# Optimization experiments

Measured on AMD Instinct MI355X. Metric: run time of the kernel, lower is better.

The kernel has to match this reference:

```python
import jax, jax.numpy as jnp
import numpy as np

B, D_IN, N_EXP, D_EXP, TOP_K = 8192, 1024, 8, 1024, 2


def setup_inputs() -> dict:
    key = jax.random.key(0)
    ks = jax.random.split(key, 6)
    s_in = 1.0 / np.sqrt(D_IN)
    s_exp = 1.0 / np.sqrt(D_EXP)
    return {
        "x": jax.random.normal(ks[0], (B, D_IN), jnp.float32),
        "gate_w": jax.random.normal(ks[1], (D_IN, N_EXP), jnp.float32) * s_in,
        "w1": jax.random.normal(ks[2], (N_EXP, D_IN, D_EXP), jnp.float32) * s_in,
        "b1": jax.random.normal(ks[3], (N_EXP, D_EXP), jnp.float32) * 0.01,
        "w2": jax.random.normal(ks[4], (N_EXP, D_EXP, D_EXP), jnp.float32) * s_exp,
        "b2": jax.random.normal(ks[5], (N_EXP, D_EXP), jnp.float32) * 0.01,
    }


def _moe(x, gate_w, w1, b1, w2, b2):
    # Gating: top-k sparse softmax over expert logits.
    gate_logits = x @ gate_w                          # (B, E)
    top_vals, top_idx = jax.lax.top_k(gate_logits, TOP_K)  # (B, K)
    # softmax over only the top-k logits == softmax of -inf-scattered logits
    top_w = jax.nn.softmax(top_vals, axis=-1)          # (B, K)
    gate_weights = jnp.zeros_like(gate_logits).at[
        jnp.arange(x.shape[0])[:, None], top_idx
    ].set(top_w)                                       # (B, E)
    # Dense all-expert MLP (matches torch.stack over experts).
    h = jax.nn.gelu(jnp.einsum("bd,edf->ebf", x, w1) + b1[:, None, :],
                    approximate=False)                 # (E, B, F)
    expert_outs = jnp.einsum("ebf,efg->ebg", h, w2) + b2[:, None, :]  # (E, B, G)
    output = jnp.einsum("be,ebg->bg", gate_weights, expert_outs)      # (B, G)
    return output, gate_weights


def reference(x, gate_w, w1, b1, w2, b2):
    return _moe(x, gate_w, w1, b1, w2, b2)
```

## Files before the change

kernel.cpp:

```cpp
#include <hip/hip_runtime.h>
#include <math.h>
#include <stdint.h>


#define NTOK   8192
#define DIN    1024
#define NEXP   8
#define DEXP   1024
#define MAXROWS 17408
#define MAXTILES 136

typedef __bf16 bf16x8_t __attribute__((ext_vector_type(8)));
typedef float f32x4 __attribute__((ext_vector_type(4)));

__device__ __forceinline__ unsigned short f2bf(float f) {
  union { float f; unsigned int u; } v; v.f = f;
  unsigned int u = v.u;
  u += 0x7fffu + ((u >> 16) & 1u);
  return (unsigned short)(u >> 16);
}

__device__ __forceinline__ float bf2f(unsigned short s) {
  union { unsigned int u; float f; } v; v.u = ((unsigned int)s) << 16;
  return v.f;
}

__device__ __forceinline__ void async16(const void* g, void* l) {
  __builtin_amdgcn_global_load_lds((const __attribute__((address_space(1))) void*)g,
                                   (__attribute__((address_space(3))) void*)l, 16, 0, 0);
}

__device__ __forceinline__ float gelu_fast(float v) {
  float u = v * (1.5957691216057308f + 0.07135481627f * v * v);
  return v * (1.0f / (1.0f + __expf(-u)));
}

__global__ __launch_bounds__(256) void gate_cast_kernel(const float* __restrict__ x,
                                                        const float* __restrict__ gw,
                                                        unsigned short* __restrict__ xbf,
                                                        float* __restrict__ outGate,
                                                        int* __restrict__ topE,
                                                        float* __restrict__ topW,
                                                        int* __restrict__ rowTok) {
  int b = blockIdx.x;
  int tid = threadIdx.x;
  if (b >= 2048) {
    int base = (b - 2048) * 1024 + tid * 4;
    *(int4*)(rowTok + base) = make_int4(-1, -1, -1, -1);
    return;
  }
  __shared__ float gwT[NEXP][1024];
  #pragma unroll
  for (int it = 0; it < 8; ++it) {
    int idx = it * 256 + tid;
    int fk = idx >> 1;
    int e0 = (idx & 1) * 4;
    float4 g = *(const float4*)(gw + fk * 8 + e0);
    gwT[e0 + 0][fk] = g.x; gwT[e0 + 1][fk] = g.y;
    gwT[e0 + 2][fk] = g.z; gwT[e0 + 3][fk] = g.w;
  }
  __syncthreads();

  int lane = tid & 63, wv = tid >> 6;
  int t = b * 4 + wv;
  const float4* xr = (const float4*)(x + (size_t)t * 1024);
  ushort4* xo = (ushort4*)(xbf + (size_t)t * 1024);
  double acc[NEXP];
  #pragma unroll
  for (int e = 0; e < NEXP; ++e) acc[e] = 0.0;
  #pragma unroll
  for (int j = 0; j < 4; ++j) {
    int q = lane + 64 * j;
    float4 v = xr[q];
    ushort4 r;
    r.x = f2bf(v.x); r.y = f2bf(v.y); r.z = f2bf(v.z); r.w = f2bf(v.w);
    xo[q] = r;
    float vv[4] = {v.x, v.y, v.z, v.w};
    #pragma unroll
    for (int e = 0; e < NEXP; ++e) {
      float4 g = *(const float4*)&gwT[e][4 * q];
      acc[e] += (double)vv[0] * (double)g.x;
      acc[e] += (double)vv[1] * (double)g.y;
      acc[e] += (double)vv[2] * (double)g.z;
      acc[e] += (double)vv[3] * (double)g.w;
    }
  }
  #pragma unroll
  for (int off = 32; off > 0; off >>= 1) {
    #pragma unroll
    for (int e = 0; e < NEXP; ++e) acc[e] += __shfl_xor(acc[e], off);
  }
  if (lane == 0) {
    int e0 = 0; double v0 = acc[0];
    #pragma unroll
    for (int e = 1; e < NEXP; ++e) if (acc[e] > v0) { v0 = acc[e]; e0 = e; }
    int e1 = -1; double v1 = -1e300;
    #pragma unroll
    for (int e = 0; e < NEXP; ++e) if (e != e0 && acc[e] > v1) { v1 = acc[e]; e1 = e; }
    float ex = expf((float)(v1 - v0));
    float inv = 1.0f / (1.0f + ex);
    float w0 = inv, w1v = ex * inv;
    float g8[8];
    #pragma unroll
    for (int e = 0; e < NEXP; ++e) g8[e] = 0.f;
    g8[e0] = w0; g8[e1] = w1v;
    float4* gp = (float4*)(outGate + t * 8);
    gp[0] = *(float4*)&g8[0];
    gp[1] = *(float4*)&g8[4];
    topE[t * 2 + 0] = e0; topE[t * 2 + 1] = e1;
    topW[t * 2 + 0] = w0; topW[t * 2 + 1] = w1v;
  }
}

__global__ __launch_bounds__(1024) void slot_kernel(const int* __restrict__ topE,
                                                    int* __restrict__ topRow,
                                                    int* __restrict__ rowTok,
                                                    int* __restrict__ tileExpert,
                                                    int* __restrict__ tileRowBase,
                                                    const float* __restrict__ w1,
                                                    unsigned short* __restrict__ w1T) {
  __shared__ int wtot[16][NEXP];
  __shared__ int wbase[16][NEXP];
  __shared__ int soff[NEXP];
  __shared__ float tile[64 * 65];
  int tid = threadIdx.x;
  if (blockIdx.x != 0) {
    int idx = blockIdx.x - 1;
    int e = idx >> 8, rest = idx & 255, kt = rest >> 4, nt = rest & 15;
    const float* s = w1 + (size_t)e * DIN * DEXP + (size_t)kt * 64 * 1024 + nt * 64;
    unsigned short* d = w1T + (size_t)e * DIN * DEXP + (size_t)nt * 64 * 1024 + kt * 64;
    int a = tid & 15, r = tid >> 4;
    float4 v = *(const float4*)(s + (size_t)r * 1024 + a * 4);
    tile[r * 65 + a * 4 + 0] = v.x;
    tile[r * 65 + a * 4 + 1] = v.y;
    tile[r * 65 + a * 4 + 2] = v.z;
    tile[r * 65 + a * 4 + 3] = v.w;
    __syncthreads();
    int nr = r;
    ushort4 o;
    o.x = f2bf(tile[(a * 4 + 0) * 65 + nr]);
    o.y = f2bf(tile[(a * 4 + 1) * 65 + nr]);
    o.z = f2bf(tile[(a * 4 + 2) * 65 + nr]);
    o.w = f2bf(tile[(a * 4 + 3) * 65 + nr]);
    *(ushort4*)(d + (size_t)nr * 1024 + a * 4) = o;
    return;
  }
  int lane = tid & 63, wv = tid >> 6;
  int a0 = tid * 16;
  unsigned long long pk = 0ull;
  int cnt[NEXP];
  #pragma unroll
  for (int e = 0; e < NEXP; ++e) cnt[e] = 0;
  for (int i = 0; i < 16; ++i) {
    int e = topE[a0 + i];
    pk |= (unsigned long long)e << (i * 4);
    cnt[e]++;
  }
  int excl[NEXP];
  #pragma unroll
  for (int e = 0; e < NEXP; ++e) {
    int v = cnt[e], sum = v;
    #pragma unroll
    for (int d = 1; d < 64; d <<= 1) {
      int u = __shfl_up(sum, d);
      if (lane >= d) sum += u;
    }
    excl[e] = sum - v;
    if (lane == 63) wtot[wv][e] = sum;
  }
  __syncthreads();
  if (tid == 0) {
    int counts[NEXP];
    for (int e = 0; e < NEXP; ++e) {
      int s = 0;
      for (int w = 0; w < 16; ++w) { wbase[w][e] = s; s += wtot[w][e]; }
      counts[e] = s;
    }
    int row = 0, tile2 = 0;
    for (int e = 0; e < NEXP; ++e) {
      soff[e] = row;
      int nt = (counts[e] + 127) >> 7;
      for (int i = 0; i < nt; ++i) { tileExpert[tile2] = e; tileRowBase[tile2] = row + i * 128; ++tile2; }
      row += nt << 7;
    }
    for (; tile2 < MAXTILES; ++tile2) tileExpert[tile2] = -1;
  }
  __syncthreads();
  int base[NEXP], run[NEXP];
  #pragma unroll
  for (int e = 0; e < NEXP; ++e) { base[e] = soff[e] + wbase[wv][e] + excl[e]; run[e] = 0; }
  for (int i = 0; i < 16; ++i) {
    int e = (int)((pk >> (i * 4)) & 7ull);
    int row = base[e] + run[e]++;
    rowTok[row] = (a0 + i) >> 1;
    topRow[a0 + i] = row;
  }
}

__global__ __launch_bounds__(256) void gemm1_kernel(const unsigned short* __restrict__ xbf,
                                                    const unsigned short* __restrict__ w1T,
                                                    const float* __restrict__ b1,
                                                    const float* __restrict__ w2,
                                                    unsigned short* __restrict__ w2T,
                                                    const int* __restrict__ tileExpert,
                                                    const int* __restrict__ tileRowBase,
                                                    const int* __restrict__ rowTok,
                                                    unsigned short* __restrict__ h) {
  __shared__ __align__(16) unsigned short sm[128 * 64 * 2];
  int bid = blockIdx.x;
  int tid = threadIdx.x;
  if (bid < 2048) {
    float* tile = (float*)sm;
    int e = bid >> 8, rest = bid & 255, kt = rest >> 4, nt = rest & 15;
    const float* s = w2 + (size_t)e * DEXP * DEXP + (size_t)kt * 64 * 1024 + nt * 64;
    unsigned short* d = w2T + (size_t)e * DEXP * DEXP + (size_t)nt * 64 * 1024 + kt * 64;
    int a = tid & 15, r0 = tid >> 4;
    #pragma unroll
    for (int p = 0; p < 4; ++p) {
      int r = r0 + p * 16;
      float4 v = *(const float4*)(s + (size_t)r * 1024 + a * 4);
      tile[r * 65 + a * 4 + 0] = v.x;
      tile[r * 65 + a * 4 + 1] = v.y;
      tile[r * 65 + a * 4 + 2] = v.z;
      tile[r * 65 + a * 4 + 3] = v.w;
    }
    __syncthreads();
    #pragma unroll
    for (int p = 0; p < 4; ++p) {
      int nr = r0 + p * 16;
      ushort4 o;
      o.x = f2bf(tile[(a * 4 + 0) * 65 + nr]);
      o.y = f2bf(tile[(a * 4 + 1) * 65 + nr]);
      o.z = f2bf(tile[(a * 4 + 2) * 65 + nr]);
      o.w = f2bf(tile[(a * 4 + 3) * 65 + nr]);
      *(ushort4*)(d + (size_t)nr * 1024 + a * 4) = o;
    }
    return;
  }
  int g = bid - 2048;
  int tileId = g % MAXTILES;
  int e = tileExpert[tileId];
  if (e < 0) return;
  int rowBase = tileRowBase[tileId];
  int n0 = (g / MAXTILES) * 128;
  unsigned short* sA = sm;
  unsigned short* sB = sm + 128 * 64;
  int lane = tid & 63, wv = tid >> 6;
  int srow = tid >> 3;
  int scolSw = (((tid & 7) ^ ((tid >> 3) & 7)) * 8);
  int tok[4];
  #pragma unroll
  for (int i = 0; i < 4; ++i) {
    int tk = rowTok[rowBase + srow + i * 32];
    tok[i] = tk < 0 ? 0 : tk;
  }
  const unsigned short* Bmat = w1T + (size_t)e * DIN * DEXP;
  int wm = ((tid >> 6) & 1) * 64, wn = (tid >> 7) * 64;
  int rsel = lane & 15, q = lane >> 4;
  int rk = rsel & 7;
  f32x4 acc[4][4] = {};
  for (int kk = 0; kk < DIN; kk += 64) {
    #pragma unroll
    for (int i = 0; i < 4; ++i) {
      int abase = __builtin_amdgcn_readfirstlane((wv * 8 + i * 32) * 128);
      async16(xbf + (size_t)tok[i] * 1024 + kk + scolSw, (char*)sm + abase);
      async16(Bmat + (size_t)(n0 + srow + i * 32) * 1024 + kk + scolSw,
              (char*)sm + abase + 16384);
    }
    __syncthreads();
    #pragma unroll
    for (int ks = 0; ks < 64; ks += 32) {
      int co = (((ks >> 3) + q) ^ rk) * 8;
      bf16x8_t af[4], bfr[4];
      #pragma unroll
      for (int mi = 0; mi < 4; ++mi)
        af[mi] = *(const bf16x8_t*)&sA[(wm + mi * 16 + rsel) * 64 + co];
      #pragma unroll
      for (int ni = 0; ni < 4; ++ni)
        bfr[ni] = *(const bf16x8_t*)&sB[(wn + ni * 16 + rsel) * 64 + co];
      #pragma unroll
      for (int mi = 0; mi < 4; ++mi)
        #pragma unroll
        for (int ni = 0; ni < 4; ++ni)
          acc[mi][ni] = __builtin_amdgcn_mfma_f32_16x16x32_bf16(af[mi], bfr[ni], acc[mi][ni], 0, 0, 0);
    }
    __syncthreads();
  }
  float b1v[4];
  int quad = lane >> 4;
  #pragma unroll
  for (int ni = 0; ni < 4; ++ni) b1v[ni] = b1[e * 1024 + n0 + wn + ni * 16 + rsel];
  #pragma unroll
  for (int mi = 0; mi < 4; ++mi)
    #pragma unroll
    for (int ni = 0; ni < 4; ++ni)
      #pragma unroll
      for (int r = 0; r < 4; ++r) {
        int m = wm + mi * 16 + quad * 4 + r;
        int n = wn + ni * 16 + rsel;
        sm[m * 128 + n] = f2bf(gelu_fast(acc[mi][ni][r] + b1v[ni]));
      }
  __syncthreads();
  #pragma unroll
  for (int i = 0; i < 8; ++i) {
    int idx = i * 2048 + tid * 8;
    int m = idx >> 7, c = idx & 127;
    int gg = rowBase + m;
    *(uint4*)(h + (size_t)gg * 1024 + n0 + c) = *(const uint4*)&sm[idx];
  }
}

__global__ __launch_bounds__(256) void gemm2_kernel(const unsigned short* __restrict__ h,
                                                    const unsigned short* __restrict__ w2T,
                                                    const float* __restrict__ b2,
                                                    const int* __restrict__ tileExpert,
                                                    const int* __restrict__ tileRowBase,
                                                    unsigned short* __restrict__ y) {
  int tileId = blockIdx.x;
  int e = tileExpert[tileId];
  if (e < 0) return;
  int rowBase = tileRowBase[tileId];
  int n0 = blockIdx.y * 128;
  __shared__ __align__(16) unsigned short sm[128 * 64 * 2];
  unsigned short* sA = sm;
  unsigned short* sB = sm + 128 * 64;
  int tid = threadIdx.x, lane = tid & 63, wv = tid >> 6;
  int srow = tid >> 3;
  int scolSw = (((tid & 7) ^ ((tid >> 3) & 7)) * 8);
  const unsigned short* Bmat = w2T + (size_t)e * DEXP * DEXP;
  int wm = ((tid >> 6) & 1) * 64, wn = (tid >> 7) * 64;
  int rsel = lane & 15, q = lane >> 4;
  int rk = rsel & 7;
  f32x4 acc[4][4] = {};
  for (int kk = 0; kk < DEXP; kk += 64) {
    #pragma unroll
    for (int i = 0; i < 4; ++i) {
      int abase = __builtin_amdgcn_readfirstlane((wv * 8 + i * 32) * 128);
      async16(h + (size_t)(rowBase + srow + i * 32) * 1024 + kk + scolSw, (char*)sm + abase);
      async16(Bmat + (size_t)(n0 + srow + i * 32) * 1024 + kk + scolSw,
              (char*)sm + abase + 16384);
    }
    __syncthreads();
    #pragma unroll
    for (int ks = 0; ks < 64; ks += 32) {
      int co = (((ks >> 3) + q) ^ rk) * 8;
      bf16x8_t af[4], bfr[4];
      #pragma unroll
      for (int mi = 0; mi < 4; ++mi)
        af[mi] = *(const bf16x8_t*)&sA[(wm + mi * 16 + rsel) * 64 + co];
      #pragma unroll
      for (int ni = 0; ni < 4; ++ni)
        bfr[ni] = *(const bf16x8_t*)&sB[(wn + ni * 16 + rsel) * 64 + co];
      #pragma unroll
      for (int mi = 0; mi < 4; ++mi)
        #pragma unroll
        for (int ni = 0; ni < 4; ++ni)
          acc[mi][ni] = __builtin_amdgcn_mfma_f32_16x16x32_bf16(af[mi], bfr[ni], acc[mi][ni], 0, 0, 0);
    }
    __syncthreads();
  }
  float b2v[4];
  int quad = lane >> 4;
  #pragma unroll
  for (int ni = 0; ni < 4; ++ni) b2v[ni] = b2[e * 1024 + n0 + wn + ni * 16 + rsel];
  #pragma unroll
  for (int mi = 0; mi < 4; ++mi)
    #pragma unroll
    for (int ni = 0; ni < 4; ++ni)
      #pragma unroll
      for (int r = 0; r < 4; ++r) {
        int m = wm + mi * 16 + quad * 4 + r;
        int n = wn + ni * 16 + rsel;
        sm[m * 128 + n] = f2bf(acc[mi][ni][r] + b2v[ni]);
      }
  __syncthreads();
  #pragma unroll
  for (int i = 0; i < 8; ++i) {
    int idx = i * 2048 + tid * 8;
    int m = idx >> 7, c = idx & 127;
    int g = rowBase + m;
    *(uint4*)(y + (size_t)g * 1024 + n0 + c) = *(const uint4*)&sm[idx];
  }
}

__global__ __launch_bounds__(256) void combine_kernel(const unsigned short* __restrict__ y,
                                                      const int* __restrict__ topRow,
                                                      const float* __restrict__ topW,
                                                      float* __restrict__ out) {
  int tid = threadIdx.x;
  int wv = tid >> 6, lane = tid & 63;
  int t = blockIdx.x * 4 + wv;
  int r0 = topRow[t * 2 + 0], r1 = topRow[t * 2 + 1];
  float w0 = topW[t * 2 + 0], w1 = topW[t * 2 + 1];
  const unsigned short* p0 = y + (size_t)r0 * 1024 + lane * 16;
  const unsigned short* p1 = y + (size_t)r1 * 1024 + lane * 16;
  float* op = out + (size_t)t * 1024 + lane * 16;
  #pragma unroll
  for (int hh = 0; hh < 2; ++hh) {
    union { uint4 v; unsigned short s[8]; } a, b;
    a.v = *(const uint4*)(p0 + hh * 8);
    b.v = *(const uint4*)(p1 + hh * 8);
    float o[8];
    #pragma unroll
    for (int j = 0; j < 8; ++j)
      o[j] = w0 * bf2f(a.s[j]) + w1 * bf2f(b.s[j]);
    *(float4*)(op + hh * 8) = *(float4*)&o[0];
    *(float4*)(op + hh * 8 + 4) = *(float4*)&o[4];
  }
}

extern "C" void kernel_launch(void* const* d_in, const int* in_sizes, int n_in,
                              void* d_out, int out_size, void* d_ws, size_t ws_size,
                              hipStream_t stream) {
  const float* x  = (const float*)d_in[0];
  const float* gw = (const float*)d_in[1];
  const float* w1 = (const float*)d_in[2];
  const float* b1 = (const float*)d_in[3];
  const float* w2 = (const float*)d_in[4];
  const float* b2 = (const float*)d_in[5];
  float* out = (float*)d_out;

  char* ws = (char*)d_ws;
  int* tileExpert  = (int*)ws;
  int* tileRowBase = tileExpert + MAXTILES;
  int* topE        = tileRowBase + MAXTILES;
  int* topRow      = topE + 16384;
  float* topW      = (float*)(topRow + 16384);
  int* rowTok      = (int*)(ws + (256 << 10));
  unsigned short* xbf  = (unsigned short*)(ws + (512 << 10));
  unsigned short* w1T  = xbf + (size_t)NTOK * DIN;
  unsigned short* w2T  = w1T + (size_t)NEXP * DIN * DEXP;
  unsigned short* hbuf = w2T + (size_t)NEXP * DEXP * DEXP;
  unsigned short* ybuf = hbuf + (size_t)MAXROWS * DEXP;

  gate_cast_kernel<<<2048 + 17, 256, 0, stream>>>(x, gw, xbf,
                                                  out + (size_t)NTOK * DEXP,
                                                  topE, topW, rowTok);
  slot_kernel<<<1 + 2048, 1024, 0, stream>>>(topE, topRow, rowTok, tileExpert,
                                             tileRowBase, w1, w1T);
  gemm1_kernel<<<2048 + MAXTILES * 8, 256, 0, stream>>>(xbf, w1T, b1, w2, w2T,
                                                        tileExpert, tileRowBase,
                                                        rowTok, hbuf);
  gemm2_kernel<<<dim3(MAXTILES, 8), 256, 0, stream>>>(hbuf, w2T, b2, tileExpert,
                                                      tileRowBase, ybuf);
  combine_kernel<<<NTOK / 4, 256, 0, stream>>>(ybuf, topRow, topW, out);
}
```

Baseline: 292.3 us.

## Use 256x256 double-buffered MFMA tiles for both expert GEMMs and move w2 cast

Replaces the two 128x128 single-buffered grouped GEMMs with one templated 512-thread kernel on 256x256 tiles. It double-buffers LDS through async global-to-LDS loads with explicit waitcnt, and raises MFMA priority with s_setprio. Expert row padding moves to 256-row tiles, and the w2 transpose/cast moves into the gate kernel so the GEMM launch does only matrix work. Bigger tiles improve reuse but pad more rows per expert and launch far fewer blocks (72x4), which can leave the GPU's compute units underused.

```diff
diff --git a/kernel.cpp b/kernel.cpp
--- a/kernel.cpp
+++ b/kernel.cpp
@@ -7,8 +7,8 @@
 #define DIN    1024
 #define NEXP   8
 #define DEXP   1024
-#define MAXROWS 17408
-#define MAXTILES 136
+#define MAXROWS 18432
+#define MAXT   72
 
 typedef __bf16 bf16x8_t __attribute__((ext_vector_type(8)));
 typedef float f32x4 __attribute__((ext_vector_type(4)));
@@ -37,19 +37,51 @@
 
 __global__ __launch_bounds__(256) void gate_cast_kernel(const float* __restrict__ x,
                                                         const float* __restrict__ gw,
+                                                        const float* __restrict__ w2,
                                                         unsigned short* __restrict__ xbf,
+                                                        unsigned short* __restrict__ w2T,
                                                         float* __restrict__ outGate,
                                                         int* __restrict__ topE,
                                                         float* __restrict__ topW,
                                                         int* __restrict__ rowTok) {
+  __shared__ __align__(16) char smem[32768];
   int b = blockIdx.x;
   int tid = threadIdx.x;
-  if (b >= 2048) {
-    int base = (b - 2048) * 1024 + tid * 4;
+  if (b >= 4096) {
+    int base = (b - 4096) * 1024 + tid * 4;
     *(int4*)(rowTok + base) = make_int4(-1, -1, -1, -1);
     return;
   }
-  __shared__ float gwT[NEXP][1024];
+  if (b >= 2048) {
+    float* tile = (float*)smem;
+    int idx = b - 2048;
+    int e = idx >> 8, rest = idx & 255, kt = rest >> 4, nt = rest & 15;
+    const float* s = w2 + (size_t)e * DEXP * DEXP + (size_t)kt * 64 * 1024 + nt * 64;
+    unsigned short* d = w2T + (size_t)e * DEXP * DEXP + (size_t)nt * 64 * 1024 + kt * 64;
+    int a = tid & 15, r0 = tid >> 4;
+    #pragma unroll
+    for (int p = 0; p < 4; ++p) {
+      int r = r0 + p * 16;
+      float4 v = *(const float4*)(s + (size_t)r * 1024 + a * 4);
+      tile[r * 65 + a * 4 + 0] = v.x;
+      tile[r * 65 + a * 4 + 1] = v.y;
+      tile[r * 65 + a * 4 + 2] = v.z;
+      tile[r * 65 + a * 4 + 3] = v.w;
+    }
+    __syncthreads();
+    #pragma unroll
+    for (int p = 0; p < 4; ++p) {
+      int nr = r0 + p * 16;
+      ushort4 o;
+      o.x = f2bf(tile[(a * 4 + 0) * 65 + nr]);
+      o.y = f2bf(tile[(a * 4 + 1) * 65 + nr]);
+      o.z = f2bf(tile[(a * 4 + 2) * 65 + nr]);
+      o.w = f2bf(tile[(a * 4 + 3) * 65 + nr]);
+      *(ushort4*)(d + (size_t)nr * 1024 + a * 4) = o;
+    }
+    return;
+  }
+  float (*gwT)[1024] = (float(*)[1024])smem;
   #pragma unroll
   for (int it = 0; it < 8; ++it) {
     int idx = it * 256 + tid;
@@ -176,14 +208,14 @@
       for (int w = 0; w < 16; ++w) { wbase[w][e] = s; s += wtot[w][e]; }
       counts[e] = s;
     }
-    int row = 0, tile2 = 0;
+    int row = 0, tl = 0;
     for (int e = 0; e < NEXP; ++e) {
       soff[e] = row;
-      int nt = (counts[e] + 127) >> 7;
-      for (int i = 0; i < nt; ++i) { tileExpert[tile2] = e; tileRowBase[tile2] = row + i * 128; ++tile2; }
-      row += nt << 7;
-    }
-    for (; tile2 < MAXTILES; ++tile2) tileExpert[tile2] = -1;
+      int nt = (counts[e] + 255) >> 8;
+      for (int i = 0; i < nt; ++i) { tileExpert[tl] = e; tileRowBase[tl] = row + i * 256; ++tl; }
+      row += nt << 8;
+    }
+    for (; tl < MAXT; ++tl) tileExpert[tl] = -1;
   }
   __syncthreads();
   int base[NEXP], run[NEXP];
@@ -197,189 +229,122 @@
   }
 }
 
-__global__ __launch_bounds__(256) void gemm1_kernel(const unsigned short* __restrict__ xbf,
-                                                    const unsigned short* __restrict__ w1T,
-                                                    const float* __restrict__ b1,
-                                                    const float* __restrict__ w2,
-                                                    unsigned short* __restrict__ w2T,
-                                                    const int* __restrict__ tileExpert,
-                                                    const int* __restrict__ tileRowBase,
-                                                    const int* __restrict__ rowTok,
-                                                    unsigned short* __restrict__ h) {
-  __shared__ __align__(16) unsigned short sm[128 * 64 * 2];
-  int bid = blockIdx.x;
+template <bool GATHER, bool GELU>
+__global__ __launch_bounds__(512, 2) void moe_gemm_kernel(
+    const unsigned short* __restrict__ Asrc,
+    const unsigned short* __restrict__ Wt,
+    const float* __restrict__ bias,
+    const int* __restrict__ tileExpert,
+    const int* __restrict__ tileRowBase,
+    const int* __restrict__ rowTok,
+    unsigned short* __restrict__ Out) {
+  int e = tileExpert[blockIdx.x];
+  if (e < 0) return;
+  int rowBase = tileRowBase[blockIdx.x];
+  int n0 = blockIdx.y * 256;
+  __shared__ __align__(16) unsigned short sm[65536];
+
   int tid = threadIdx.x;
-  if (bid < 2048) {
-    float* tile = (float*)sm;
-    int e = bid >> 8, rest = bid & 255, kt = rest >> 4, nt = rest & 15;
-    const float* s = w2 + (size_t)e * DEXP * DEXP + (size_t)kt * 64 * 1024 + nt * 64;
-    unsigned short* d = w2T + (size_t)e * DEXP * DEXP + (size_t)nt * 64 * 1024 + kt * 64;
-    int a = tid & 15, r0 = tid >> 4;
+  int lane = tid & 63, wq = tid >> 6;
+  int wr = wq >> 2, wc = wq & 3;
+  int rsel = lane & 15, qq = (lane >> 4) & 3, rk = rsel & 7;
+  int sid = tid >> 3, sch = tid & 7;
+  int swz8 = (sch ^ (sid & 7)) * 8;
+
+  int arow[4];
+  #pragma unroll
+  for (int j = 0; j < 4; ++j) {
+    int r = rowBase + j * 64 + sid;
+    if (GATHER) { int tk = rowTok[r]; arow[j] = tk < 0 ? 0 : tk; }
+    else arow[j] = r;
+  }
+  const unsigned short* Bsrc = Wt + (size_t)e * 1024 * 1024;
+
+  auto stage = [&](int T) {
+    int kk_ = T * 64;
+    int sel_ = (T & 1) * 32768;
+    #pragma unroll
+    for (int j = 0; j < 4; ++j) {
+      int ab = __builtin_amdgcn_readfirstlane(sel_ + j * 8192 + wq * 1024);
+      async16(Asrc + (size_t)arow[j] * 1024 + kk_ + swz8, (char*)sm + ab);
+      async16(Bsrc + (size_t)(n0 + j * 64 + sid) * 1024 + kk_ + swz8,
+              (char*)sm + 65536 + ab);
+    }
+  };
+
+  f32x4 acc[8][4] = {};
+
+  stage(0);
+  stage(1);
+  asm volatile("s_waitcnt vmcnt(8)" ::: "memory");
+  __builtin_amdgcn_s_barrier();
+
+  for (int t = 0; t < 16; ++t) {
+    int sel = (t & 1) * 32768;
+    const unsigned short* sA = (const unsigned short*)((const char*)sm + sel);
+    const unsigned short* sB = (const unsigned short*)((const char*)sm + 65536 + sel);
+    bf16x8_t bfr[4][2];
+    #pragma unroll
+    for (int ni = 0; ni < 4; ++ni)
+      #pragma unroll
+      for (int ks = 0; ks < 2; ++ks)
+        bfr[ni][ks] = *(const bf16x8_t*)
+            &sB[(wc * 64 + ni * 16 + rsel) * 64 + ((qq + 4 * ks) ^ rk) * 8];
     #pragma unroll
     for (int p = 0; p < 4; ++p) {
-      int r = r0 + p * 16;
-      float4 v = *(const float4*)(s + (size_t)r * 1024 + a * 4);
-      tile[r * 65 + a * 4 + 0] = v.x;
-      tile[r * 65 + a * 4 + 1] = v.y;
-      tile[r * 65 + a * 4 + 2] = v.z;
-      tile[r * 65 + a * 4 + 3] = v.w;
-    }
-    __syncthreads();
-    #pragma unroll
-    for (int p = 0; p < 4; ++p) {
-      int nr = r0 + p * 16;
-      ushort4 o;
-      o.x = f2bf(tile[(a * 4 + 0) * 65 + nr]);
-      o.y = f2bf(tile[(a * 4 + 1) * 65 + nr]);
-      o.z = f2bf(tile[(a * 4 + 2) * 65 + nr]);
-      o.w = f2bf(tile[(a * 4 + 3) * 65 + nr]);
-      *(ushort4*)(d + (size_t)nr * 1024 + a * 4) = o;
-    }
-    return;
-  }
-  int g = bid - 2048;
-  int tileId = g % MAXTILES;
-  int e = tileExpert[tileId];
-  if (e < 0) return;
-  int rowBase = tileRowBase[tileId];
-  int n0 = (g / MAXTILES) * 128;
-  unsigned short* sA = sm;
-  unsigned short* sB = sm + 128 * 64;
-  int lane = tid & 63, wv = tid >> 6;
-  int srow = tid >> 3;
-  int scolSw = (((tid & 7) ^ ((tid >> 3) & 7)) * 8);
-  int tok[4];
-  #pragma unroll
-  for (int i = 0; i < 4; ++i) {
-    int tk = rowTok[rowBase + srow + i * 32];
-    tok[i] = tk < 0 ? 0 : tk;
-  }
-  const unsigned short* Bmat = w1T + (size_t)e * DIN * DEXP;
-  int wm = ((tid >> 6) & 1) * 64, wn = (tid >> 7) * 64;
-  int rsel = lane & 15, q = lane >> 4;
-  int rk = rsel & 7;
-  f32x4 acc[4][4] = {};
-  for (int kk = 0; kk < DIN; kk += 64) {
-    #pragma unroll
-    for (int i = 0; i < 4; ++i) {
-      int abase = __builtin_amdgcn_readfirstlane((wv * 8 + i * 32) * 128);
-      async16(xbf + (size_t)tok[i] * 1024 + kk + scolSw, (char*)sm + abase);
-      async16(Bmat + (size_t)(n0 + srow + i * 32) * 1024 + kk + scolSw,
-              (char*)sm + abase + 16384);
-    }
-    __syncthreads();
-    #pragma unroll
-    for (int ks = 0; ks < 64; ks += 32) {
-      int co = (((ks >> 3) + q) ^ rk) * 8;
-      bf16x8_t af[4], bfr[4];
+      bf16x8_t af[2][2];
       #pragma unroll
-      for (int mi = 0; mi < 4; ++mi)
-        af[mi] = *(const bf16x8_t*)&sA[(wm + mi * 16 + rsel) * 64 + co];
+      for (int d = 0; d < 2; ++d)
+        #pragma unroll
+        for (int ks = 0; ks < 2; ++ks)
+          af[d][ks] = *(const bf16x8_t*)
+              &sA[(wr * 128 + (p * 2 + d) * 16 + rsel) * 64 + ((qq + 4 * ks) ^ rk) * 8];
+      __builtin_amdgcn_s_barrier();
+      __builtin_amdgcn_s_setprio(1);
       #pragma unroll
-      for (int ni = 0; ni < 4; ++ni)
-        bfr[ni] = *(const bf16x8_t*)&sB[(wn + ni * 16 + rsel) * 64 + co];
-      #pragma unroll
-      for (int mi = 0; mi < 4; ++mi)
+      for (int d = 0; d < 2; ++d)
         #pragma unroll
         for (int ni = 0; ni < 4; ++ni)
-          acc[mi][ni] = __builtin_amdgcn_mfma_f32_16x16x32_bf16(af[mi], bfr[ni], acc[mi][ni], 0, 0, 0);
-    }
-    __syncthreads();
-  }
-  float b1v[4];
-  int quad = lane >> 4;
-  #pragma unroll
-  for (int ni = 0; ni < 4; ++ni) b1v[ni] = b1[e * 1024 + n0 + wn + ni * 16 + rsel];
-  #pragma unroll
-  for (int mi = 0; mi < 4; ++mi)
+          #pragma unroll
+          for (int ks = 0; ks < 2; ++ks)
+            acc[p * 2 + d][ni] = __builtin_amdgcn_mfma_f32_16x16x32_bf16(
+                af[d][ks], bfr[ni][ks], acc[p * 2 + d][ni], 0, 0, 0);
+      __builtin_amdgcn_s_setprio(0);
+      __builtin_amdgcn_s_barrier();
+    }
+    if (t + 2 < 16) {
+      stage(t + 2);
+      asm volatile("s_waitcnt vmcnt(8)" ::: "memory");
+    } else {
+      asm volatile("s_waitcnt vmcnt(0)" ::: "memory");
+    }
+    __builtin_amdgcn_s_barrier();
+  }
+
+  __syncthreads();
+  float bv[4];
+  #pragma unroll
+  for (int ni = 0; ni < 4; ++ni)
+    bv[ni] = bias[e * 1024 + n0 + wc * 64 + ni * 16 + rsel];
+  #pragma unroll
+  for (int mi = 0; mi < 8; ++mi)
     #pragma unroll
     for (int ni = 0; ni < 4; ++ni)
       #pragma unroll
       for (int r = 0; r < 4; ++r) {
-        int m = wm + mi * 16 + quad * 4 + r;
-        int n = wn + ni * 16 + rsel;
-        sm[m * 128 + n] = f2bf(gelu_fast(acc[mi][ni][r] + b1v[ni]));
+        int m = wr * 128 + mi * 16 + qq * 4 + r;
+        int n = wc * 64 + ni * 16 + rsel;
+        float v = acc[mi][ni][r] + bv[ni];
+        if (GELU) v = gelu_fast(v);
+        sm[m * 256 + n] = f2bf(v);
       }
   __syncthreads();
   #pragma unroll
-  for (int i = 0; i < 8; ++i) {
-    int idx = i * 2048 + tid * 8;
-    int m = idx >> 7, c = idx & 127;
-    int gg = rowBase + m;
-    *(uint4*)(h + (size_t)gg * 1024 + n0 + c) = *(const uint4*)&sm[idx];
-  }
-}
-
-__global__ __launch_bounds__(256) void gemm2_kernel(const unsigned short* __restrict__ h,
-                                                    const unsigned short* __restrict__ w2T,
-                                                    const float* __restrict__ b2,
-                                                    const int* __restrict__ tileExpert,
-                                                    const int* __restrict__ tileRowBase,
-                                                    unsigned short* __restrict__ y) {
-  int tileId = blockIdx.x;
-  int e = tileExpert[tileId];
-  if (e < 0) return;
-  int rowBase = tileRowBase[tileId];
-  int n0 = blockIdx.y * 128;
-  __shared__ __align__(16) unsigned short sm[128 * 64 * 2];
-  unsigned short* sA = sm;
-  unsigned short* sB = sm + 128 * 64;
-  int tid = threadIdx.x, lane = tid & 63, wv = tid >> 6;
-  int srow = tid >> 3;
-  int scolSw = (((tid & 7) ^ ((tid >> 3) & 7)) * 8);
-  const unsigned short* Bmat = w2T + (size_t)e * DEXP * DEXP;
-  int wm = ((tid >> 6) & 1) * 64, wn = (tid >> 7) * 64;
-  int rsel = lane & 15, q = lane >> 4;
-  int rk = rsel & 7;
-  f32x4 acc[4][4] = {};
-  for (int kk = 0; kk < DEXP; kk += 64) {
-    #pragma unroll
-    for (int i = 0; i < 4; ++i) {
-      int abase = __builtin_amdgcn_readfirstlane((wv * 8 + i * 32) * 128);
-      async16(h + (size_t)(rowBase + srow + i * 32) * 1024 + kk + scolSw, (char*)sm + abase);
-      async16(Bmat + (size_t)(n0 + srow + i * 32) * 1024 + kk + scolSw,
-              (char*)sm + abase + 16384);
-    }
-    __syncthreads();
-    #pragma unroll
-    for (int ks = 0; ks < 64; ks += 32) {
-      int co = (((ks >> 3) + q) ^ rk) * 8;
-      bf16x8_t af[4], bfr[4];
-      #pragma unroll
-      for (int mi = 0; mi < 4; ++mi)
-        af[mi] = *(const bf16x8_t*)&sA[(wm + mi * 16 + rsel) * 64 + co];
-      #pragma unroll
-      for (int ni = 0; ni < 4; ++ni)
-        bfr[ni] = *(const bf16x8_t*)&sB[(wn + ni * 16 + rsel) * 64 + co];
-      #pragma unroll
-      for (int mi = 0; mi < 4; ++mi)
-        #pragma unroll
-        for (int ni = 0; ni < 4; ++ni)
-          acc[mi][ni] = __builtin_amdgcn_mfma_f32_16x16x32_bf16(af[mi], bfr[ni], acc[mi][ni], 0, 0, 0);
-    }
-    __syncthreads();
-  }
-  float b2v[4];
-  int quad = lane >> 4;
-  #pragma unroll
-  for (int ni = 0; ni < 4; ++ni) b2v[ni] = b2[e * 1024 + n0 + wn + ni * 16 + rsel];
-  #pragma unroll
-  for (int mi = 0; mi < 4; ++mi)
-    #pragma unroll
-    for (int ni = 0; ni < 4; ++ni)
-      #pragma unroll
-      for (int r = 0; r < 4; ++r) {
-        int m = wm + mi * 16 + quad * 4 + r;
-        int n = wn + ni * 16 + rsel;
-        sm[m * 128 + n] = f2bf(acc[mi][ni][r] + b2v[ni]);
-      }
-  __syncthreads();
-  #pragma unroll
-  for (int i = 0; i < 8; ++i) {
-    int idx = i * 2048 + tid * 8;
-    int m = idx >> 7, c = idx & 127;
-    int g = rowBase + m;
-    *(uint4*)(y + (size_t)g * 1024 + n0 + c) = *(const uint4*)&sm[idx];
+  for (int i = 0; i < 16; ++i) {
+    int idx = i * 8192 + tid * 16;
+    int m = idx >> 9, cb = idx & 511;
+    *(uint4*)(Out + (size_t)(rowBase + m) * 1024 + n0 + (cb >> 1)) =
+        *(const uint4*)((const char*)sm + idx);
   }
 }
 
@@ -422,8 +387,8 @@
 
   char* ws = (char*)d_ws;
   int* tileExpert  = (int*)ws;
-  int* tileRowBase = tileExpert + MAXTILES;
-  int* topE        = tileRowBase + MAXTILES;
+  int* tileRowBase = tileExpert + MAXT;
+  int* topE        = tileRowBase + MAXT;
   int* topRow      = topE + 16384;
   float* topW      = (float*)(topRow + 16384);
   int* rowTok      = (int*)(ws + (256 << 10));
@@ -433,15 +398,14 @@
   unsigned short* hbuf = w2T + (size_t)NEXP * DEXP * DEXP;
   unsigned short* ybuf = hbuf + (size_t)MAXROWS * DEXP;
 
-  gate_cast_kernel<<<2048 + 17, 256, 0, stream>>>(x, gw, xbf,
-                                                  out + (size_t)NTOK * DEXP,
-                                                  topE, topW, rowTok);
+  gate_cast_kernel<<<2048 + 2048 + 18, 256, 0, stream>>>(x, gw, w2, xbf, w2T,
+                                                         out + (size_t)NTOK * DEXP,
+                                                         topE, topW, rowTok);
   slot_kernel<<<1 + 2048, 1024, 0, stream>>>(topE, topRow, rowTok, tileExpert,
                                              tileRowBase, w1, w1T);
-  gemm1_kernel<<<2048 + MAXTILES * 8, 256, 0, stream>>>(xbf, w1T, b1, w2, w2T,
-                                                        tileExpert, tileRowBase,
-                                                        rowTok, hbuf);
-  gemm2_kernel<<<dim3(MAXTILES, 8), 256, 0, stream>>>(hbuf, w2T, b2, tileExpert,
-                                                      tileRowBase, ybuf);
+  moe_gemm_kernel<true, true><<<dim3(MAXT, 4), 512, 0, stream>>>(
+      xbf, w1T, b1, tileExpert, tileRowBase, rowTok, hbuf);
+  moe_gemm_kernel<false, false><<<dim3(MAXT, 4), 512, 0, stream>>>(
+      hbuf, w2T, b2, tileExpert, tileRowBase, rowTok, ybuf);
   combine_kernel<<<NTOK / 4, 256, 0, stream>>>(ybuf, topRow, topW, out);
 }
```

New measurement: 322.9 us. +10.5%, slower.
